# Optimization experiments

Measured on AMD Instinct MI355X. Metric: run time of the kernel, lower is better.

Reference implementation:

```python
import jax, jax.numpy as jnp
import numpy as np
from jax import lax

B, C1, IN_CH, OUT_CH, H1, W1 = 2, 64, 128, 64, 128, 128
BN_EPS = 1e-5


def conv3x3(x, w, b=None):
    # x: (N,C,H,W), w: (O,I,3,3), padding=1, stride=1 (matches nn.Conv2d)
    y = lax.conv_general_dilated(x, w, (1, 1), ((1, 1), (1, 1)),
                                 dimension_numbers=('NCHW', 'OIHW', 'NCHW'))
    return y if b is None else y + b[None, :, None, None]


def bn_relu(x, g, b):
    # training-mode BatchNorm2d (batch statistics over N,H,W) followed by ReLU
    m = x.mean((0, 2, 3), keepdims=True)
    v = x.var((0, 2, 3), keepdims=True)
    return jax.nn.relu((x - m) * lax.rsqrt(v + BN_EPS) * g[None, :, None, None]
                       + b[None, :, None, None])


def deform_offset(x, off_w):
    # ConvOffset2D: learn 2 offsets per pixel per channel, bilinear-gather input.
    Bc, C, H, W = x.shape
    offsets = conv3x3(x, off_w)                      # (B, 2C, H, W)
    off = offsets.reshape(Bc * C, H, W, 2)           # same flat reinterpretation as torch .view
    xf = x.reshape(Bc * C, H, W)
    gy, gx = jnp.meshgrid(jnp.arange(H, dtype=x.dtype),
                          jnp.arange(W, dtype=x.dtype), indexing='ij')
    cy = jnp.clip(off[..., 0] + gy, 0.0, H - 1)      # clamp per-axis like th_batch_map_coordinates
    cx = jnp.clip(off[..., 1] + gx, 0.0, W - 1)
    y0f, x0f = jnp.floor(cy), jnp.floor(cx)
    y0 = y0f.astype(jnp.int32); y1 = jnp.ceil(cy).astype(jnp.int32)
    x0 = x0f.astype(jnp.int32); x1c = jnp.ceil(cx).astype(jnp.int32)
    bidx = jnp.arange(Bc * C)[:, None, None]
    v00 = xf[bidx, y0, x0]; v10 = xf[bidx, y1, x0]
    v01 = xf[bidx, y0, x1c]; v11 = xf[bidx, y1, x1c]
    wy = cy - y0f; wx = cx - x0f
    vt = v00 + (v10 - v00) * wy                      # interp along H
    vb = v01 + (v11 - v01) * wy
    return (vt + (vb - vt) * wx).reshape(Bc, C, H, W)


def setup_inputs() -> dict:
    key = jax.random.key(0)
    ks = jax.random.split(key, 8)
    f = jnp.float32
    x1 = jax.random.normal(ks[0], (B, C1, H1, W1), f)
    x2 = jax.random.normal(ks[1], (B, C1, 2 * H1, 2 * W1), f)
    up_w = jax.random.normal(ks[2], (C1, C1, 2, 2), f) * 0.05   # torch IOHW layout
    up_b = jnp.zeros((C1,), f)
    off_w = jax.random.normal(ks[3], (2 * IN_CH, IN_CH, 3, 3), f) * 0.01  # init_normal_stddev
    c1_w = jax.random.normal(ks[4], (OUT_CH, IN_CH, 3, 3), f) * 0.05
    c1_b = jnp.zeros((OUT_CH,), f)
    g1 = jnp.ones((OUT_CH,), f); b1 = jnp.zeros((OUT_CH,), f)
    c2_w = jax.random.normal(ks[5], (OUT_CH, OUT_CH, 3, 3), f) * 0.05
    c2_b = jnp.zeros((OUT_CH,), f)
    g2 = jnp.ones((OUT_CH,), f); b2 = jnp.zeros((OUT_CH,), f)
    return dict(x1=x1, x2=x2, up_w=up_w, up_b=up_b, off_w=off_w,
                c1_w=c1_w, c1_b=c1_b, g1=g1, b1=b1,
                c2_w=c2_w, c2_b=c2_b, g2=g2, b2=b2)


def reference(x1, x2, up_w, up_b, off_w, c1_w, c1_b, g1, b1, c2_w, c2_b, g2, b2):
    # ConvTranspose2d(k=2, s=2): each input pixel expands to a 2x2 block
    Bx, Ci, H, W = x1.shape
    up = jnp.einsum('bihw,iokl->bohkwl', x1, up_w).reshape(Bx, up_w.shape[1], 2 * H, 2 * W)
    up = up + up_b[None, :, None, None]
    # pad skip connection to match (zero here; kept for faithfulness; torch pads W by diffX, H by diffY)
    dX = up.shape[2] - x2.shape[2]
    dY = up.shape[3] - x2.shape[3]
    x2p = jnp.pad(x2, ((0, 0), (0, 0), (dY // 2, dY // 2), (dX // 2, dX // 2)))
    xcat = jnp.concatenate([x2p, up], axis=1)        # (B, IN_CH, 2H, 2W)
    xd = deform_offset(xcat, off_w)
    h = bn_relu(conv3x3(xd, c1_w, c1_b), g1, b1)
    return bn_relu(conv3x3(h, c2_w, c2_b), g2, b2)
```

## Files before the change

### kernel.cpp

```cpp
#include <hip/hip_runtime.h>
#include <hip/hip_bf16.h>


typedef short short8 __attribute__((ext_vector_type(8)));
typedef short short4v __attribute__((ext_vector_type(4)));
typedef float f32x4 __attribute__((ext_vector_type(4)));

__device__ unsigned char g_ws[197u << 20] __attribute__((aligned(256)));
__device__ float g_st[256];

#define OFF_XCAT 0u
#define OFF_OFF  (36u << 20)
#define OFF_XD   (100u << 20)
#define OFF_C1O  (132u << 20)
#define OFF_H1   (148u << 20)
#define OFF_C2O  (164u << 20)
#define OFF_WO   (180u << 20)
#define OFF_W1   ((180u << 20) + 589824u)
#define OFF_W2   ((180u << 20) + 737280u)
#define OFF_XPU  (181u << 20)

#define XROW 264
#define XRSH (XROW * 128)

__device__ __forceinline__ float b2f(__hip_bfloat16 v) { return __bfloat162float(v); }
__device__ __forceinline__ short f2b(float v) {
  __hip_bfloat16 h = __float2bfloat16(v); short s; __builtin_memcpy(&s, &h, 2); return s;
}
__device__ __forceinline__ float s2f(short s) {
  __hip_bfloat16 h; __builtin_memcpy(&h, &s, 2); return __bfloat162float(h);
}
__device__ __forceinline__ void gload_lds16(const void* g, void* l) {
  __builtin_amdgcn_global_load_lds(
      (const __attribute__((address_space(1))) void*)g,
      (__attribute__((address_space(3))) void*)l, 16, 0, 0);
}

__global__ __launch_bounds__(256)
void k_prep(const float* __restrict__ offw, const float* __restrict__ c1w,
            const float* __restrict__ c2w) {
  const int fid = blockIdx.x * 256 + threadIdx.x;
  if (blockIdx.x == 0) g_st[threadIdx.x] = 0.f;
  __hip_bfloat16* Wo = (__hip_bfloat16*)(g_ws + OFF_WO);
  __hip_bfloat16* W1 = (__hip_bfloat16*)(g_ws + OFF_W1);
  __hip_bfloat16* W2 = (__hip_bfloat16*)(g_ws + OFF_W2);
  if (fid < 294912) {
    int ic = fid & 127, rest = fid >> 7, oc = rest & 255, tap = rest >> 8;
    Wo[fid] = __float2bfloat16(offw[(oc * 128 + ic) * 9 + tap]);
  } else if (fid < 368640) {
    int l = fid - 294912;
    int ic = l & 127, rest = l >> 7, oc = rest & 63, tap = rest >> 6;
    W1[l] = __float2bfloat16(c1w[(oc * 128 + ic) * 9 + tap]);
  } else {
    int l = fid - 368640;
    int ic = l & 63, rest = l >> 6, oc = rest & 63, tap = rest >> 6;
    W2[l] = __float2bfloat16(c2w[(oc * 64 + ic) * 9 + tap]);
  }
}

__global__ __launch_bounds__(256)
void k_zhalo() {
  short* xp = (short*)(g_ws + OFF_XCAT);
  const int u = blockIdx.x * 256 + threadIdx.x;
  const int cg = u & 15;
  const int rest = u >> 4;
  const int p = rest % 2576, b = rest / 2576;
  int row, col;
  if (p < 264) { row = 0; col = p; }
  else if (p < 528) { row = 257; col = p - 264; }
  else { int q = p - 528; row = 1 + (q >> 3); int cs = q & 7; col = cs ? 256 + cs : 0; }
  short8 z = {};
  *(short8*)(xp + (((size_t)(b * 258) + row) * XROW + col) * 128 + cg * 8) = z;
}

__global__ __launch_bounds__(256)
void k_xpose(const float* __restrict__ x2) {
  __shared__ short T[256][72];
  const int t = threadIdx.x;
  const int h = blockIdx.x & 255, b = blockIdx.x >> 8;
  const float* src = x2 + (size_t)(b * 64) * 65536 + h * 256;
  for (int rep = 0; rep < 64; ++rep) {
    int flat = rep * 256 + t, c = flat >> 8, w = flat & 255;
    T[w][c] = f2b(src[(size_t)c * 65536 + w]);
  }
  __syncthreads();
  short* xcat = (short*)(g_ws + OFF_XCAT) +
                (((size_t)(b * 258) + h + 1) * XROW + 1) * 128;
  for (int rep = 0; rep < 8; ++rep) {
    int unit = rep * 256 + t;
    int w = unit >> 3, cg = unit & 7;
    *(short8*)(xcat + (size_t)w * 128 + cg * 8) = *(short8*)(&T[w][cg * 8]);
  }
}

__global__ __launch_bounds__(256)
void k_upmfma(const float* __restrict__ x1, const float* __restrict__ up_w,
              const float* __restrict__ up_b) {
  __shared__ short W4[4][64][66];
  __shared__ short X[64][68];
  __shared__ short U[2][128][66];
  __shared__ float BS[64];
  const int t = threadIdx.x;
  const int half = blockIdx.x & 1, hs = (blockIdx.x >> 1) & 127, b = blockIdx.x >> 8;
  for (int rep = 0; rep < 64; ++rep) {
    int flat = rep * 256 + t;
    int i = flat >> 8, rest = flat & 255, o = rest >> 2, kl = rest & 3;
    W4[kl][o][i] = f2b(up_w[flat]);
  }
  if (t < 64) BS[t] = up_b[t];
  const float* x1b = x1 + (size_t)(b * 64) * 16384 + hs * 128 + half * 64;
  for (int rep = 0; rep < 16; ++rep) {
    int flat = rep * 256 + t;
    int i = flat >> 6, ws = flat & 63;
    X[ws][i] = f2b(x1b[(size_t)i * 16384 + ws]);
  }
  __syncthreads();
  const int wv = t >> 6, lane = t & 63, l15 = lane & 15, quad = lane >> 4;
  short8 bf[2];
#pragma unroll
  for (int ks = 0; ks < 2; ++ks)
    bf[ks] = *(const short8*)(&X[wv * 16 + l15][ks * 32 + quad * 8]);
#pragma unroll
  for (int combo = 0; combo < 4; ++combo) {
    const int k = combo >> 1, l = combo & 1;
    f32x4 acc[4] = {};
#pragma unroll
    for (int nt = 0; nt < 4; ++nt)
#pragma unroll
      for (int ks = 0; ks < 2; ++ks) {
        short8 af = *(const short8*)(&W4[combo][nt * 16 + l15][ks * 32 + quad * 8]);
        acc[nt] = __builtin_amdgcn_mfma_f32_16x16x32_bf16(af, bf[ks], acc[nt], 0, 0, 0);
      }
    const int wl = 2 * (wv * 16 + l15) + l;
#pragma unroll
    for (int nt = 0; nt < 4; ++nt) {
      short4v s;
#pragma unroll
      for (int r = 0; r < 4; ++r) s[r] = f2b(acc[nt][r] + BS[nt * 16 + quad * 4 + r]);
      *(short4v*)(&U[k][wl][nt * 16 + quad * 4]) = s;
    }
  }
  __syncthreads();
  short* xcat = (short*)(g_ws + OFF_XCAT);
  short* xpu = (short*)(g_ws + OFF_XPU);
  for (int rep = 0; rep < 8; ++rep) {
    int unit = rep * 256 + t;
    int k = unit >> 10, wl = (unit >> 3) & 127, cg = unit & 7;
    int h = 2 * hs + k, w = half * 128 + wl;
    *(short8*)(xcat + (((size_t)(b * 258) + h + 1) * XROW + w + 1) * 128 + 64 + cg * 8) =
        *(short8*)(&U[k][wl][cg * 8]);
  }
  for (int rep = 0; rep < 8; ++rep) {
    int unit = rep * 256 + t;
    int o = unit >> 5, k = (unit >> 4) & 1, wg = unit & 15;
    int h = 2 * hs + k;
    short8 v;
#pragma unroll
    for (int j = 0; j < 8; ++j) v[j] = U[k][wg * 8 + j][o];
    *(short8*)(xpu + (size_t)(b * 64 + o) * 65536 + h * 256 + half * 128 + wg * 8) = v;
  }
}

__global__ __launch_bounds__(512, 2)
void k_offconv() {
  __shared__ short Bs[3 * 264 * 64];
  __shared__ short As0[256 * 32];
  __shared__ short As1[256 * 32];
  const short* X = (const short*)(g_ws + OFF_XCAT);
  const __hip_bfloat16* W = (const __hip_bfloat16*)(g_ws + OFF_WO);
  const int t = threadIdx.x;
  const int vb = (int)((blockIdx.x & 7) * 64 + (blockIdx.x >> 3));
  const int h = vb & 255, b = vb >> 8;
  const int wid = t >> 6, lane = t & 63, l15 = lane & 15, quad = lane >> 4;
  const int ocbase = (wid & 1) * 128;
  const int pxb = (wid >> 1) * 64;
  const int lpx = lane >> 3, lcg = lane & 7;
  const short* bsrc = X + (((size_t)(b * 258) + h) * XROW + lpx) * 128 + (lcg ^ (lpx & 7)) * 8;
  const int loc = lane >> 2, lcg4 = lane & 3;
  const __hip_bfloat16* asrc = W + (size_t)loc * 128 + (lcg4 ^ ((loc + (loc >> 2)) & 3)) * 8;
  const int ax = (quad ^ ((l15 + (l15 >> 2)) & 3)) << 3;
  const int abase = (ocbase + l15) * 32 + ax;
  f32x4 acc[8][4] = {};

#define STAGE_A(TAP, ICS, P, APTR)                                                  \
  {                                                                                 \
    _Pragma("unroll")                                                               \
    for (int k = 0; k < 2; ++k) {                                                   \
      int u = wid * 2 + k;                                                          \
      gload_lds16(asrc + ((size_t)(TAP) * 256 + u * 16) * 128 + (P) * 64 + (ICS) * 32, \
                  &APTR[u * 512]);                                                  \
    }                                                                               \
  }

  for (int p = 0; p < 2; ++p) {
    if (p) __syncthreads();
    for (int u = wid; u < 99; u += 8) {
      int r = u / 33, g = u - r * 33;
      gload_lds16(bsrc + (size_t)r * XRSH + g * 1024 + p * 64, &Bs[(r * 264 + g * 8) * 64]);
    }
    STAGE_A(0, 0, p, As0);
    STAGE_A(0, 1, p, As1);
    __syncthreads();
    for (int tap = 0; tap < 9; ++tap) {
      const int ky = tap / 3, kx = tap - 3 * ky;
      const short* srow = &Bs[(ky * 264 + pxb + l15 + kx) * 64];
      const int sx = ((l15 + kx) & 7) << 3;
      {
        short8 a[8], bf[4];
#pragma unroll
        for (int ot = 0; ot < 8; ++ot) a[ot] = *(const short8*)(As0 + abase + ot * 512);
#pragma unroll
        for (int pt = 0; pt < 4; ++pt)
          bf[pt] = *(const short8*)(srow + pt * 1024 + ((quad * 8) ^ sx));
        __syncthreads();
        if (tap < 8) STAGE_A(tap + 1, 0, p, As0);
#pragma unroll
        for (int ot = 0; ot < 8; ++ot)
#pragma unroll
          for (int pt = 0; pt < 4; ++pt)
            acc[ot][pt] = __builtin_amdgcn_mfma_f32_16x16x32_bf16(a[ot], bf[pt], acc[ot][pt], 0, 0, 0);
      }
      {
        short8 a[8], bf[4];
#pragma unroll
        for (int ot = 0; ot < 8; ++ot) a[ot] = *(const short8*)(As1 + abase + ot * 512);
#pragma unroll
        for (int pt = 0; pt < 4; ++pt)
          bf[pt] = *(const short8*)(srow + pt * 1024 + ((32 + quad * 8) ^ sx));
        __syncthreads();
        if (tap < 8) STAGE_A(tap + 1, 1, p, As1);
#pragma unroll
        for (int ot = 0; ot < 8; ++ot)
#pragma unroll
          for (int pt = 0; pt < 4; ++pt)
            acc[ot][pt] = __builtin_amdgcn_mfma_f32_16x16x32_bf16(a[ot], bf[pt], acc[ot][pt], 0, 0, 0);
      }
    }
  }
  __hip_bfloat16* out = (__hip_bfloat16*)(g_ws + OFF_OFF);
#pragma unroll
  for (int ot = 0; ot < 8; ++ot)
#pragma unroll
    for (int pt = 0; pt < 4; ++pt)
#pragma unroll
      for (int r = 0; r < 4; ++r) {
        int oc = ocbase + ot * 16 + quad * 4 + r;
        int px = pxb + pt * 16 + l15;
        out[(((size_t)(b * 256 + oc)) * 256 + h) * 256 + px] =
            __float2bfloat16(acc[ot][pt][r]);
      }
#undef STAGE_A
}

template <int IC>
__global__ __launch_bounds__(256, 2)
void k_convmfma(size_t xoff, size_t woff, const float* __restrict__ bias, size_t ooff) {
  const __hip_bfloat16* X = (const __hip_bfloat16*)(g_ws + xoff);
  const __hip_bfloat16* W = (const __hip_bfloat16*)(g_ws + woff);
  const int t = threadIdx.x;
  const int wv = t >> 6, lane = t & 63, l15 = lane & 15, quad = lane >> 4;
  const int h = blockIdx.x & 255, b = blockIdx.x >> 8;
  const int pixw = wv * 64;
  const int KS = IC / 32;
  f32x4 acc[4][4] = {};
  for (int tap = 0; tap < 9; ++tap) {
    const int ky = tap / 3, kx = tap - 3 * ky;
    const int row = h + ky - 1;
    const bool rowok = (unsigned)row < 256u;
    int pix[4]; bool pok[4];
#pragma unroll
    for (int pt = 0; pt < 4; ++pt) {
      pix[pt] = pixw + pt * 16 + l15 + kx - 1;
      pok[pt] = rowok && (unsigned)pix[pt] < 256u;
    }
    const __hip_bfloat16* wtap = W + ((size_t)tap * 64 + l15) * IC + quad * 8;
    const __hip_bfloat16* xrow = X + (((size_t)(b * 256) + row) * 256) * IC + quad * 8;
#pragma unroll
    for (int ics = 0; ics < KS; ++ics) {
      short8 a[4];
#pragma unroll
      for (int ot = 0; ot < 4; ++ot)
        a[ot] = *(const short8*)(wtap + ot * 16 * IC + ics * 32);
      short8 bf[4];
#pragma unroll
      for (int pt = 0; pt < 4; ++pt) {
        short8 z = {};
        bf[pt] = pok[pt] ? *(const short8*)(xrow + (size_t)pix[pt] * IC + ics * 32) : z;
      }
#pragma unroll
      for (int ot = 0; ot < 4; ++ot)
#pragma unroll
        for (int pt = 0; pt < 4; ++pt)
          acc[ot][pt] = __builtin_amdgcn_mfma_f32_16x16x32_bf16(a[ot], bf[pt], acc[ot][pt], 0, 0, 0);
    }
  }
  __hip_bfloat16* out = (__hip_bfloat16*)(g_ws + ooff);
#pragma unroll
  for (int ot = 0; ot < 4; ++ot) {
    int oc0 = ot * 16 + quad * 4;
    float bv[4];
#pragma unroll
    for (int r = 0; r < 4; ++r) bv[r] = bias[oc0 + r];
#pragma unroll
    for (int pt = 0; pt < 4; ++pt) {
      int px = pixw + pt * 16 + l15;
      short4v s;
#pragma unroll
      for (int r = 0; r < 4; ++r) s[r] = f2b(acc[ot][pt][r] + bv[r]);
      *(short4v*)(out + ((((size_t)(b * 256) + h) * 256 + px) * 64 + oc0)) = s;
    }
  }
}

__global__ __launch_bounds__(256, 4)
void k_gather(const float* __restrict__ x2) {
  __shared__ short G[256 * 66];
  const __hip_bfloat16* off = (const __hip_bfloat16*)(g_ws + OFF_OFF);
  const __hip_bfloat16* xpu = (const __hip_bfloat16*)(g_ws + OFF_XPU);
  short* xd = (short*)(g_ws + OFF_XD);
  const int t = threadIdx.x;
  const int half = blockIdx.x & 1;
  const int hh = (blockIdx.x >> 1) & 255, b = blockIdx.x >> 9;
  const int hp = 2 * (hh & 127) + (t >> 7);
  const int w0e = 2 * (t & 127);
  const int chb = hh >> 7;
  const int c0 = half * 64;
  const float fh = (float)hh, fw = (float)t;
  const __hip_bfloat16* offb = off + ((size_t)(b * 256) * 256 + hp) * 256 + w0e +
                               (size_t)(2 * c0 + chb) * 65536;
  if (half == 0) {
    const float* x2b = x2 + (size_t)b * 64 * 65536;
    for (int g4 = 0; g4 < 16; ++g4) {
      unsigned ovv[4];
#pragma unroll
      for (int j = 0; j < 4; ++j)
        ovv[j] = *(const unsigned*)(offb + (size_t)(2 * (g4 * 4 + j)) * 65536);
#pragma unroll
      for (int j = 0; j < 4; ++j) {
        const int crel = g4 * 4 + j;
        unsigned ov = ovv[j];
        float oy = __uint_as_float((ov & 0xffffu) << 16);
        float ox = __uint_as_float((ov >> 16) << 16);
        float cy = fminf(fmaxf(oy + fh, 0.f), 255.f);
        float cx = fminf(fmaxf(ox + fw, 0.f), 255.f);
        float y0f = floorf(cy), x0f = floorf(cx);
        int y0 = (int)y0f, x0 = (int)x0f;
        int y1 = (int)ceilf(cy), x1 = (int)ceilf(cx);
        const float* pl = x2b + (size_t)crel * 65536;
        float v00 = pl[y0 * 256 + x0], v10 = pl[y1 * 256 + x0];
        float v01 = pl[y0 * 256 + x1], v11 = pl[y1 * 256 + x1];
        float wy = cy - y0f, wx = cx - x0f;
        float vt = v00 + (v10 - v00) * wy;
        float vb = v01 + (v11 - v01) * wy;
        G[t * 66 + crel] = f2b(vt + (vb - vt) * wx);
      }
    }
  } else {
    const __hip_bfloat16* xub = xpu + (size_t)b * 64 * 65536;
    for (int g4 = 0; g4 < 16; ++g4) {
      unsigned ovv[4];
#pragma unroll
      for (int j = 0; j < 4; ++j)
        ovv[j] = *(const unsigned*)(offb + (size_t)(2 * (g4 * 4 + j)) * 65536);
#pragma unroll
      for (int j = 0; j < 4; ++j) {
        const int crel = g4 * 4 + j;
        unsigned ov = ovv[j];
        float oy = __uint_as_float((ov & 0xffffu) << 16);
        float ox = __uint_as_float((ov >> 16) << 16);
        float cy = fminf(fmaxf(oy + fh, 0.f), 255.f);
        float cx = fminf(fmaxf(ox + fw, 0.f), 255.f);
        float y0f = floorf(cy), x0f = floorf(cx);
        int y0 = (int)y0f, x0 = (int)x0f;
        int y1 = (int)ceilf(cy), x1 = (int)ceilf(cx);
        const __hip_bfloat16* pl = xub + (size_t)crel * 65536;
        float v00 = b2f(pl[y0 * 256 + x0]), v10 = b2f(pl[y1 * 256 + x0]);
        float v01 = b2f(pl[y0 * 256 + x1]), v11 = b2f(pl[y1 * 256 + x1]);
        float wy = cy - y0f, wx = cx - x0f;
        float vt = v00 + (v10 - v00) * wy;
        float vb = v01 + (v11 - v01) * wy;
        G[t * 66 + crel] = f2b(vt + (vb - vt) * wx);
      }
    }
  }
  __syncthreads();
  const size_t dst = (size_t)(b * 256 + hh) * 256 * 128 + c0;
  for (int it = 0; it < 8; ++it) {
    int g = it * 256 + t;
    *(short8*)(xd + dst + (size_t)(g >> 3) * 128 + (g & 7) * 8) =
        *(short8*)(&G[(g >> 3) * 66 + (g & 7) * 8]);
  }
}

template <int SO>
__global__ __launch_bounds__(256)
void k_stats(size_t xoff) {
  const __hip_bfloat16* x = (const __hip_bfloat16*)(g_ws + xoff);
  __shared__ float P[256][9], P2[256][9];
  const int t = threadIdx.x;
  const int c0 = (t & 7) * 8;
  const int pg = t >> 3;
  float s[8] = {}, s2[8] = {};
  const size_t base = (size_t)blockIdx.x * 512;
  for (int i = 0; i < 16; ++i) {
    size_t p = base + pg + (size_t)i * 32;
    short8 v = *(const short8*)(x + p * 64 + c0);
#pragma unroll
    for (int j = 0; j < 8; ++j) {
      float f = s2f(v[j]);
      s[j] += f; s2[j] = fmaf(f, f, s2[j]);
    }
  }
#pragma unroll
  for (int j = 0; j < 8; ++j) { P[t][j] = s[j]; P2[t][j] = s2[j]; }
  __syncthreads();
  if (t < 64) {
    int cg = t >> 3, j = t & 7;
    float a = 0.f, a2 = 0.f;
    for (int kk = 0; kk < 32; ++kk) { a += P[kk * 8 + cg][j]; a2 += P2[kk * 8 + cg][j]; }
    atomicAdd(&g_st[SO + t], a);
    atomicAdd(&g_st[SO + 64 + t], a2);
  }
}

template <int SO>
__global__ void k_finstat() {
  int c = threadIdx.x;
  if (c < 64) {
    float m = g_st[SO + c] * (1.f / 131072.f);
    float v = g_st[SO + 64 + c] * (1.f / 131072.f) - m * m;
    g_st[SO + c] = m;
    g_st[SO + 64 + c] = rsqrtf(v + 1e-5f);
  }
}

__global__ __launch_bounds__(256)
void k_bnrelu1(const float* __restrict__ g, const float* __restrict__ be) {
  const __hip_bfloat16* x = (const __hip_bfloat16*)(g_ws + OFF_C1O);
  __hip_bfloat16* o = (__hip_bfloat16*)(g_ws + OFF_H1);
  size_t idx = ((size_t)blockIdx.x * 256 + threadIdx.x) * 8;
  int c0 = (int)(idx & 63);
  short8 v = *(const short8*)(x + idx);
  short8 r;
#pragma unroll
  for (int j = 0; j < 8; ++j) {
    int c = c0 + j;
    float f = (s2f(v[j]) - g_st[c]) * g_st[64 + c] * g[c] + be[c];
    r[j] = f2b(fmaxf(f, 0.f));
  }
  *(short8*)(o + idx) = r;
}

__global__ __launch_bounds__(256)
void k_bnrelu2(const float* __restrict__ g, const float* __restrict__ be,
               float* __restrict__ dout) {
  __shared__ float T[64 * 257];
  const __hip_bfloat16* x = (const __hip_bfloat16*)(g_ws + OFF_C2O);
  const int t = threadIdx.x;
  const int h = blockIdx.x & 255, b = blockIdx.x >> 8;
  const __hip_bfloat16* px = x + (((size_t)(b * 256) + h) * 256 + t) * 64;
#pragma unroll
  for (int cg = 0; cg < 8; ++cg) {
    short8 v = *(const short8*)(px + cg * 8);
#pragma unroll
    for (int j = 0; j < 8; ++j) {
      int c = cg * 8 + j;
      float f = (s2f(v[j]) - g_st[128 + c]) * g_st[192 + c] * g[c] + be[c];
      T[c * 257 + t] = fmaxf(f, 0.f);
    }
  }
  __syncthreads();
  for (int rep = 0; rep < 64; ++rep) {
    int flat = rep * 256 + t, c = flat >> 8, w = flat & 255;
    dout[(((size_t)(b * 64 + c)) * 256 + h) * 256 + w] = T[c * 257 + w];
  }
}

extern "C" void kernel_launch(void* const* d_in, const int* in_sizes, int n_in,
                              void* d_out, int out_size, void* d_ws, size_t ws_size,
                              hipStream_t stream) {
  const bool ok = (n_in == 13) &&
                  in_sizes[0] == 2097152 && in_sizes[1] == 8388608 &&
                  in_sizes[2] == 16384 && in_sizes[3] == 64 &&
                  in_sizes[4] == 294912 && in_sizes[5] == 73728 &&
                  in_sizes[9] == 36864 && out_size == 8388608;
  if (!ok) { hipMemsetAsync(d_out, 0x46, (size_t)out_size * 2, stream); return; }

  const float* x1   = (const float*)d_in[0];
  const float* x2   = (const float*)d_in[1];
  const float* up_w = (const float*)d_in[2];
  const float* up_b = (const float*)d_in[3];
  const float* offw = (const float*)d_in[4];
  const float* c1w  = (const float*)d_in[5];
  const float* c1b  = (const float*)d_in[6];
  const float* g1   = (const float*)d_in[7];
  const float* b1   = (const float*)d_in[8];
  const float* c2w  = (const float*)d_in[9];
  const float* c2b  = (const float*)d_in[10];
  const float* g2   = (const float*)d_in[11];
  const float* b2   = (const float*)d_in[12];

  k_prep<<<1584, 256, 0, stream>>>(offw, c1w, c2w);
  k_zhalo<<<322, 256, 0, stream>>>();
  k_xpose<<<512, 256, 0, stream>>>(x2);
  k_upmfma<<<512, 256, 0, stream>>>(x1, up_w, up_b);
  k_offconv<<<512, 512, 0, stream>>>();
  k_gather<<<1024, 256, 0, stream>>>(x2);
  k_convmfma<128><<<512, 256, 0, stream>>>(OFF_XD, OFF_W1, c1b, OFF_C1O);
  k_stats<0><<<256, 256, 0, stream>>>(OFF_C1O);
  k_finstat<0><<<1, 64, 0, stream>>>();
  k_bnrelu1<<<4096, 256, 0, stream>>>(g1, b1);
  k_convmfma<64><<<512, 256, 0, stream>>>(OFF_H1, OFF_W2, c2b, OFF_C2O);
  k_stats<128><<<256, 256, 0, stream>>>(OFF_C2O);
  k_finstat<128><<<1, 64, 0, stream>>>();
  k_bnrelu2<<<512, 256, 0, stream>>>(g2, b2, (float*)d_out);

  (void)d_ws; (void)ws_size;
}
```

Measured before the change: 397.2 us.

## Fuse BN stats into LDS-staged conv kernels with padded halo layouts

Rewrites the two 3x3 convs to stage input rows and weight slices in LDS through global_load_lds, using swizzled slots and double-buffered weights, over zero-padded halo buffers so no bounds checks are needed. The conv epilogue now accumulates per-channel sum and sum-of-squares, which removes the separate stats and finalize kernels. The BN scale and shift are computed inside the bnrelu kernels, and halo zeroing is folded into the prep kernel. Together these cut launches and a full re-read of each conv output, at the cost of extra syncthreads per tap and atomics in the epilogue.

```diff
diff --git a/kernel.cpp b/kernel.cpp
--- a/kernel.cpp
+++ b/kernel.cpp
@@ -6,19 +6,19 @@
 typedef short short4v __attribute__((ext_vector_type(4)));
 typedef float f32x4 __attribute__((ext_vector_type(4)));
 
-__device__ unsigned char g_ws[197u << 20] __attribute__((aligned(256)));
+__device__ unsigned char g_ws[201u << 20] __attribute__((aligned(256)));
 __device__ float g_st[256];
 
 #define OFF_XCAT 0u
 #define OFF_OFF  (36u << 20)
 #define OFF_XD   (100u << 20)
-#define OFF_C1O  (132u << 20)
-#define OFF_H1   (148u << 20)
-#define OFF_C2O  (164u << 20)
-#define OFF_WO   (180u << 20)
-#define OFF_W1   ((180u << 20) + 589824u)
-#define OFF_W2   ((180u << 20) + 737280u)
-#define OFF_XPU  (181u << 20)
+#define OFF_C1O  (134u << 20)
+#define OFF_H1   (150u << 20)
+#define OFF_C2O  (168u << 20)
+#define OFF_WO   (184u << 20)
+#define OFF_W1   ((184u << 20) + 589824u)
+#define OFF_W2   ((184u << 20) + 737280u)
+#define OFF_XPU  (185u << 20)
 
 #define XROW 264
 #define XRSH (XROW * 128)
@@ -34,6 +34,18 @@
   __builtin_amdgcn_global_load_lds(
       (const __attribute__((address_space(1))) void*)g,
       (__attribute__((address_space(3))) void*)l, 16, 0, 0);
+}
+
+__device__ __forceinline__ void halo_zero(short* base, int C, int cshift, int u) {
+  const int cg = u & ((1 << cshift) - 1);
+  const int rest = u >> cshift;
+  const int p = rest % 2576, b = rest / 2576;
+  int row, col;
+  if (p < 264) { row = 0; col = p; }
+  else if (p < 528) { row = 257; col = p - 264; }
+  else { int q = p - 528; row = 1 + (q >> 3); int cs = q & 7; col = cs ? 256 + cs : 0; }
+  short8 z = {};
+  *(short8*)(base + (((size_t)(b * 258) + row) * XROW + col) * C + cg * 8) = z;
 }
 
 __global__ __launch_bounds__(256)
@@ -51,26 +63,16 @@
     int l = fid - 294912;
     int ic = l & 127, rest = l >> 7, oc = rest & 63, tap = rest >> 6;
     W1[l] = __float2bfloat16(c1w[(oc * 128 + ic) * 9 + tap]);
-  } else {
+  } else if (fid < 405504) {
     int l = fid - 368640;
     int ic = l & 63, rest = l >> 6, oc = rest & 63, tap = rest >> 6;
     W2[l] = __float2bfloat16(c2w[(oc * 64 + ic) * 9 + tap]);
-  }
-}
-
-__global__ __launch_bounds__(256)
-void k_zhalo() {
-  short* xp = (short*)(g_ws + OFF_XCAT);
-  const int u = blockIdx.x * 256 + threadIdx.x;
-  const int cg = u & 15;
-  const int rest = u >> 4;
-  const int p = rest % 2576, b = rest / 2576;
-  int row, col;
-  if (p < 264) { row = 0; col = p; }
-  else if (p < 528) { row = 257; col = p - 264; }
-  else { int q = p - 528; row = 1 + (q >> 3); int cs = q & 7; col = cs ? 256 + cs : 0; }
-  short8 z = {};
-  *(short8*)(xp + (((size_t)(b * 258) + row) * XROW + col) * 128 + cg * 8) = z;
+  } else {
+    int u = fid - 405504;
+    if (u < 82432) halo_zero((short*)(g_ws + OFF_XCAT), 128, 4, u);
+    else if (u < 164864) halo_zero((short*)(g_ws + OFF_XD), 128, 4, u - 82432);
+    else halo_zero((short*)(g_ws + OFF_H1), 64, 3, u - 164864);
+  }
 }
 
 __global__ __launch_bounds__(256)
@@ -252,64 +254,94 @@
 #undef STAGE_A
 }
 
-template <int IC>
+template <int IC, int SO>
 __global__ __launch_bounds__(256, 2)
-void k_convmfma(size_t xoff, size_t woff, const float* __restrict__ bias, size_t ooff) {
-  const __hip_bfloat16* X = (const __hip_bfloat16*)(g_ws + xoff);
+void k_conv(size_t xoff, size_t woff, const float* __restrict__ bias, size_t ooff) {
+  __shared__ short Bs[3 * 272 * 32];
+  __shared__ short As[2 * 2048];
+  __shared__ float SB[128];
+  const short* X = (const short*)(g_ws + xoff);
   const __hip_bfloat16* W = (const __hip_bfloat16*)(g_ws + woff);
   const int t = threadIdx.x;
-  const int wv = t >> 6, lane = t & 63, l15 = lane & 15, quad = lane >> 4;
-  const int h = blockIdx.x & 255, b = blockIdx.x >> 8;
-  const int pixw = wv * 64;
-  const int KS = IC / 32;
+  const int vb = (int)((blockIdx.x & 7) * 64 + (blockIdx.x >> 3));
+  const int h = vb & 255, b = vb >> 8;
+  const int wid = t >> 6, lane = t & 63, l15 = lane & 15, quad = lane >> 4;
+  const int pxb = wid * 64;
+  if (t < 128) SB[t] = 0.f;
+  const int lpx = lane >> 2, lc = lane & 3;
+  const int fl = (lpx + (lpx >> 2)) & 3;
+  const short* bsrc = X + (((size_t)(b * 258) + h) * XROW + lpx) * IC + (lc ^ fl) * 8;
+  const __hip_bfloat16* asrc = W + (size_t)lpx * IC + (lc ^ fl) * 8;
+  const int aslot = (quad ^ ((l15 + (l15 >> 2)) & 3)) << 3;
   f32x4 acc[4][4] = {};
-  for (int tap = 0; tap < 9; ++tap) {
-    const int ky = tap / 3, kx = tap - 3 * ky;
-    const int row = h + ky - 1;
-    const bool rowok = (unsigned)row < 256u;
-    int pix[4]; bool pok[4];
-#pragma unroll
-    for (int pt = 0; pt < 4; ++pt) {
-      pix[pt] = pixw + pt * 16 + l15 + kx - 1;
-      pok[pt] = rowok && (unsigned)pix[pt] < 256u;
-    }
-    const __hip_bfloat16* wtap = W + ((size_t)tap * 64 + l15) * IC + quad * 8;
-    const __hip_bfloat16* xrow = X + (((size_t)(b * 256) + row) * 256) * IC + quad * 8;
-#pragma unroll
-    for (int ics = 0; ics < KS; ++ics) {
-      short8 a[4];
+  const int KP = IC / 32;
+  for (int ph = 0; ph < KP; ++ph) {
+    for (int u = wid; u < 51; u += 4) {
+      int r = u / 17, g = u - r * 17;
+      gload_lds16(bsrc + ((size_t)r * XROW + g * 16) * IC + ph * 32,
+                  &Bs[(r * 272 + g * 16) * 32]);
+    }
+    gload_lds16(asrc + (size_t)(wid * 16) * IC + ph * 32, &As[wid * 512]);
+    __syncthreads();
+    for (int tap = 0; tap < 9; ++tap) {
+      short* Ac = &As[(tap & 1) * 2048];
+      short* An = &As[((tap & 1) ^ 1) * 2048];
+      if (tap < 8)
+        gload_lds16(asrc + ((size_t)((tap + 1) * 64) + wid * 16) * IC + ph * 32,
+                    &An[wid * 512]);
+      const int ky = tap / 3, kx = tap - 3 * ky;
+      short8 a[4], bf[4];
 #pragma unroll
       for (int ot = 0; ot < 4; ++ot)
-        a[ot] = *(const short8*)(wtap + ot * 16 * IC + ics * 32);
-      short8 bf[4];
-#pragma unroll
-      for (int pt = 0; pt < 4; ++pt) {
-        short8 z = {};
-        bf[pt] = pok[pt] ? *(const short8*)(xrow + (size_t)pix[pt] * IC + ics * 32) : z;
-      }
+        a[ot] = *(const short8*)(&Ac[(ot * 16 + l15) * 32 + aslot]);
+      const int s = l15 + kx;
+      const int bslot = (quad ^ ((s + (s >> 2)) & 3)) << 3;
+#pragma unroll
+      for (int pt = 0; pt < 4; ++pt)
+        bf[pt] = *(const short8*)(&Bs[(ky * 272 + pxb + pt * 16 + s) * 32 + bslot]);
 #pragma unroll
       for (int ot = 0; ot < 4; ++ot)
 #pragma unroll
         for (int pt = 0; pt < 4; ++pt)
           acc[ot][pt] = __builtin_amdgcn_mfma_f32_16x16x32_bf16(a[ot], bf[pt], acc[ot][pt], 0, 0, 0);
+      __syncthreads();
     }
   }
   __hip_bfloat16* out = (__hip_bfloat16*)(g_ws + ooff);
 #pragma unroll
   for (int ot = 0; ot < 4; ++ot) {
-    int oc0 = ot * 16 + quad * 4;
-    float bv[4];
+    const int oc0 = ot * 16 + quad * 4;
+    float bv[4], sa[4] = {}, sa2[4] = {};
 #pragma unroll
     for (int r = 0; r < 4; ++r) bv[r] = bias[oc0 + r];
 #pragma unroll
     for (int pt = 0; pt < 4; ++pt) {
-      int px = pixw + pt * 16 + l15;
-      short4v s;
-#pragma unroll
-      for (int r = 0; r < 4; ++r) s[r] = f2b(acc[ot][pt][r] + bv[r]);
-      *(short4v*)(out + ((((size_t)(b * 256) + h) * 256 + px) * 64 + oc0)) = s;
-    }
-  }
+      const int px = pxb + pt * 16 + l15;
+      short4v sv;
+#pragma unroll
+      for (int r = 0; r < 4; ++r) {
+        float f = acc[ot][pt][r] + bv[r];
+        sv[r] = f2b(f);
+        sa[r] += f;
+        sa2[r] = fmaf(f, f, sa2[r]);
+      }
+      *(short4v*)(out + ((((size_t)(b * 256) + h) * 256 + px) * 64 + oc0)) = sv;
+    }
+#pragma unroll
+    for (int r = 0; r < 4; ++r) {
+      float sv1 = sa[r], sv2 = sa2[r];
+      for (int d = 1; d < 16; d <<= 1) {
+        sv1 += __shfl_xor(sv1, d);
+        sv2 += __shfl_xor(sv2, d);
+      }
+      if (l15 == 0) {
+        atomicAdd(&SB[oc0 + r], sv1);
+        atomicAdd(&SB[64 + oc0 + r], sv2);
+      }
+    }
+  }
+  __syncthreads();
+  if (t < 128) atomicAdd(&g_st[SO + t], SB[t]);
 }
 
 __global__ __launch_bounds__(256, 4)
@@ -384,7 +416,7 @@
     }
   }
   __syncthreads();
-  const size_t dst = (size_t)(b * 256 + hh) * 256 * 128 + c0;
+  const size_t dst = (((size_t)(b * 258) + hh + 1) * XROW + 1) * 128 + c0;
   for (int it = 0; it < 8; ++it) {
     int g = it * 256 + t;
     *(short8*)(xd + dst + (size_t)(g >> 3) * 128 + (g & 7) * 8) =
@@ -392,72 +424,52 @@
   }
 }
 
-template <int SO>
-__global__ __launch_bounds__(256)
-void k_stats(size_t xoff) {
-  const __hip_bfloat16* x = (const __hip_bfloat16*)(g_ws + xoff);
-  __shared__ float P[256][9], P2[256][9];
-  const int t = threadIdx.x;
-  const int c0 = (t & 7) * 8;
-  const int pg = t >> 3;
-  float s[8] = {}, s2[8] = {};
-  const size_t base = (size_t)blockIdx.x * 512;
-  for (int i = 0; i < 16; ++i) {
-    size_t p = base + pg + (size_t)i * 32;
-    short8 v = *(const short8*)(x + p * 64 + c0);
-#pragma unroll
-    for (int j = 0; j < 8; ++j) {
-      float f = s2f(v[j]);
-      s[j] += f; s2[j] = fmaf(f, f, s2[j]);
-    }
-  }
-#pragma unroll
-  for (int j = 0; j < 8; ++j) { P[t][j] = s[j]; P2[t][j] = s2[j]; }
-  __syncthreads();
-  if (t < 64) {
-    int cg = t >> 3, j = t & 7;
-    float a = 0.f, a2 = 0.f;
-    for (int kk = 0; kk < 32; ++kk) { a += P[kk * 8 + cg][j]; a2 += P2[kk * 8 + cg][j]; }
-    atomicAdd(&g_st[SO + t], a);
-    atomicAdd(&g_st[SO + 64 + t], a2);
-  }
-}
-
-template <int SO>
-__global__ void k_finstat() {
-  int c = threadIdx.x;
-  if (c < 64) {
-    float m = g_st[SO + c] * (1.f / 131072.f);
-    float v = g_st[SO + 64 + c] * (1.f / 131072.f) - m * m;
-    g_st[SO + c] = m;
-    g_st[SO + 64 + c] = rsqrtf(v + 1e-5f);
-  }
-}
-
 __global__ __launch_bounds__(256)
 void k_bnrelu1(const float* __restrict__ g, const float* __restrict__ be) {
+  __shared__ float A[64], Bc[64];
   const __hip_bfloat16* x = (const __hip_bfloat16*)(g_ws + OFF_C1O);
-  __hip_bfloat16* o = (__hip_bfloat16*)(g_ws + OFF_H1);
-  size_t idx = ((size_t)blockIdx.x * 256 + threadIdx.x) * 8;
-  int c0 = (int)(idx & 63);
-  short8 v = *(const short8*)(x + idx);
-  short8 r;
-#pragma unroll
-  for (int j = 0; j < 8; ++j) {
-    int c = c0 + j;
-    float f = (s2f(v[j]) - g_st[c]) * g_st[64 + c] * g[c] + be[c];
-    r[j] = f2b(fmaxf(f, 0.f));
-  }
-  *(short8*)(o + idx) = r;
+  short* o = (short*)(g_ws + OFF_H1);
+  const int t = threadIdx.x;
+  const int h = blockIdx.x & 255, b = blockIdx.x >> 8;
+  if (t < 64) {
+    float m = g_st[t] * (1.f / 131072.f);
+    float v = g_st[64 + t] * (1.f / 131072.f) - m * m;
+    float iv = rsqrtf(v + 1e-5f) * g[t];
+    A[t] = iv;
+    Bc[t] = be[t] - m * iv;
+  }
+  __syncthreads();
+  const __hip_bfloat16* px = x + (((size_t)(b * 256) + h) * 256 + t) * 64;
+  short* op = o + (((size_t)(b * 258) + h + 1) * XROW + t + 1) * 64;
+#pragma unroll
+  for (int cg = 0; cg < 8; ++cg) {
+    short8 v = *(const short8*)(px + cg * 8);
+    short8 r;
+#pragma unroll
+    for (int j = 0; j < 8; ++j) {
+      int c = cg * 8 + j;
+      r[j] = f2b(fmaxf(s2f(v[j]) * A[c] + Bc[c], 0.f));
+    }
+    *(short8*)(op + cg * 8) = r;
+  }
 }
 
 __global__ __launch_bounds__(256)
 void k_bnrelu2(const float* __restrict__ g, const float* __restrict__ be,
                float* __restrict__ dout) {
   __shared__ float T[64 * 257];
+  __shared__ float A[64], Bc[64];
   const __hip_bfloat16* x = (const __hip_bfloat16*)(g_ws + OFF_C2O);
   const int t = threadIdx.x;
   const int h = blockIdx.x & 255, b = blockIdx.x >> 8;
+  if (t < 64) {
+    float m = g_st[128 + t] * (1.f / 131072.f);
+    float v = g_st[192 + t] * (1.f / 131072.f) - m * m;
+    float iv = rsqrtf(v + 1e-5f) * g[t];
+    A[t] = iv;
+    Bc[t] = be[t] - m * iv;
+  }
+  __syncthreads();
   const __hip_bfloat16* px = x + (((size_t)(b * 256) + h) * 256 + t) * 64;
 #pragma unroll
   for (int cg = 0; cg < 8; ++cg) {
@@ -465,8 +477,7 @@
 #pragma unroll
     for (int j = 0; j < 8; ++j) {
       int c = cg * 8 + j;
-      float f = (s2f(v[j]) - g_st[128 + c]) * g_st[192 + c] * g[c] + be[c];
-      T[c * 257 + t] = fmaxf(f, 0.f);
+      T[c * 257 + t] = fmaxf(s2f(v[j]) * A[c] + Bc[c], 0.f);
     }
   }
   __syncthreads();
@@ -500,19 +511,14 @@
   const float* g2   = (const float*)d_in[11];
   const float* b2   = (const float*)d_in[12];
 
-  k_prep<<<1584, 256, 0, stream>>>(offw, c1w, c2w);
-  k_zhalo<<<322, 256, 0, stream>>>();
+  k_prep<<<2389, 256, 0, stream>>>(offw, c1w, c2w);
   k_xpose<<<512, 256, 0, stream>>>(x2);
   k_upmfma<<<512, 256, 0, stream>>>(x1, up_w, up_b);
   k_offconv<<<512, 512, 0, stream>>>();
   k_gather<<<1024, 256, 0, stream>>>(x2);
-  k_convmfma<128><<<512, 256, 0, stream>>>(OFF_XD, OFF_W1, c1b, OFF_C1O);
-  k_stats<0><<<256, 256, 0, stream>>>(OFF_C1O);
-  k_finstat<0><<<1, 64, 0, stream>>>();
-  k_bnrelu1<<<4096, 256, 0, stream>>>(g1, b1);
-  k_convmfma<64><<<512, 256, 0, stream>>>(OFF_H1, OFF_W2, c2b, OFF_C2O);
-  k_stats<128><<<256, 256, 0, stream>>>(OFF_C2O);
-  k_finstat<128><<<1, 64, 0, stream>>>();
+  k_conv<128, 0><<<512, 256, 0, stream>>>(OFF_XD, OFF_W1, c1b, OFF_C1O);
+  k_bnrelu1<<<512, 256, 0, stream>>>(g1, b1);
+  k_conv<64, 128><<<512, 256, 0, stream>>>(OFF_H1, OFF_W2, c2b, OFF_C2O);
   k_bnrelu2<<<512, 256, 0, stream>>>(g2, b2, (float*)d_out);
 
   (void)d_ws; (void)ws_size;
```

New measurement: 340.6 us (median of 2 runs). -14.2%, faster.
